# Kernel optimization log

Measured on AMD Instinct MI355X. Metric: run time of the kernel, lower is better.

Reference implementation:

```python
import jax, jax.numpy as jnp
import numpy as np

K = 3    # kernel size
PAD = 1  # padding ('same' for stride 1)


def _quantize(t):
    # dynamic per-tensor absmax int8 quantization
    s = jnp.max(jnp.abs(t)) / 127.0
    q = jnp.clip(jnp.round(t / s), -128, 127).astype(jnp.int32)
    return q, s


def _patches(x, k, pad):
    # im2col: [B,C,H,W] -> [B, C*k*k, OH, OW] (flatten order C, kh, kw matches
    # weight.reshape(Cout, Cin*k*k)); stride 1.
    B, C, H, W = x.shape
    xp = jnp.pad(x, ((0, 0), (0, 0), (pad, pad), (pad, pad)))
    cols = [xp[:, :, i:i + H, j:j + W] for i in range(k) for j in range(k)]
    return jnp.stack(cols, axis=2).reshape(B, C * k * k, H, W)


def setup_inputs() -> dict:
    key = jax.random.key(0)
    k1, k2, k3 = jax.random.split(key, 3)
    B, Cin, H, W, Cout = 8, 64, 14, 14, 64
    x = jax.random.normal(k1, (B, Cin, H, W), dtype=jnp.float32)
    weight = jax.random.normal(k2, (Cout, Cin, K, K), dtype=jnp.float32) * 0.05
    bias = jax.random.normal(k3, (Cout,), dtype=jnp.float32) * 0.1
    # LUT of the (approximate) int8 multiplier: lut[a+128, b+128] ~= a*b
    q = jnp.arange(256, dtype=jnp.float32) - 128.0
    lut = q[:, None] * q[None, :]                                   # [256,256]
    # gradient LUT: [...,0] = d(prod)/da ~= b ; [...,1] = d(prod)/db ~= a
    gradient_lut = jnp.stack(
        [jnp.broadcast_to(q[None, :], (256, 256)),
         jnp.broadcast_to(q[:, None], (256, 256))], axis=-1)        # [256,256,2]
    return {"x": x, "weight": weight, "bias": bias,
            "lut": lut, "gradient_lut": gradient_lut}


def reference(x, weight, bias, lut, gradient_lut):
    Cout = weight.shape[0]
    p = _patches(x, K, PAD)                  # [B, Kdim, OH, OW]
    qx, sx = _quantize(p)
    qw, sw = _quantize(weight.reshape(Cout, -1))   # [Cout, Kdim]
    # per-tap LUT lookup: idx[b,o,k,oh,ow] = (qx+128)*256 + (qw+128)
    idx = (qx + 128)[:, None] * 256 + (qw + 128)[None, :, :, None, None]
    vals = lut.reshape(-1)[idx]              # [B, Cout, Kdim, OH, OW]
    out = sx * sw * vals.sum(axis=2) + bias[None, :, None, None]
    return out
```

## Files before the change

### kernel.cpp

```cpp
#include <hip/hip_runtime.h>

#define NB   8
#define CIN  64
#define HW   14
#define COUT 64
#define NX   (NB*CIN*HW*HW)
#define NW   (COUT*CIN*9)


__global__ __launch_bounds__(256) void absmax_kernel(const float* __restrict__ x,
                                                     const float* __restrict__ w,
                                                     float* __restrict__ part) {
    const int bid = blockIdx.x, tid = threadIdx.x;
    float m = 0.f;
    if (bid < 64) {
        const float4* p = (const float4*)x;
        for (int i = bid * 256 + tid; i < NX / 4; i += 64 * 256) {
            float4 v = p[i];
            m = fmaxf(m, fmaxf(fmaxf(fabsf(v.x), fabsf(v.y)),
                               fmaxf(fabsf(v.z), fabsf(v.w))));
        }
    } else {
        const float4* p = (const float4*)w;
        for (int i = (bid - 64) * 256 + tid; i < NW / 4; i += 16 * 256) {
            float4 v = p[i];
            m = fmaxf(m, fmaxf(fmaxf(fabsf(v.x), fabsf(v.y)),
                               fmaxf(fabsf(v.z), fabsf(v.w))));
        }
    }
    #pragma unroll
    for (int off = 32; off; off >>= 1)
        m = fmaxf(m, __shfl_down(m, off, 64));
    __shared__ float lds[4];
    if ((tid & 63) == 0) lds[tid >> 6] = m;
    __syncthreads();
    if (tid == 0)
        part[bid] = fmaxf(fmaxf(lds[0], lds[1]), fmaxf(lds[2], lds[3]));
}

__device__ __forceinline__ float reduce_part(const float* __restrict__ part, int lo, int hi) {
    float m = 0.f;
    for (int i = lo; i < hi; ++i) m = fmaxf(m, part[i]);
    return m;
}

__device__ __forceinline__ signed char quant1(float v, float s) {
    int q = (int)rintf(v / s);
    return (signed char)min(127, max(-128, q));
}

__device__ __forceinline__ int dot4(int a, int b, int acc) {
#if __has_builtin(__builtin_amdgcn_sdot4)
    return __builtin_amdgcn_sdot4(a, b, acc, false);
#else
    acc += (int)(signed char)(a)       * (int)(signed char)(b);
    acc += (int)(signed char)(a >> 8)  * (int)(signed char)(b >> 8);
    acc += (int)(signed char)(a >> 16) * (int)(signed char)(b >> 16);
    acc += (a >> 24)                   * (b >> 24);
    return acc;
#endif
}

__global__ __launch_bounds__(512) void fused_kernel(const float* __restrict__ x,
                                                    const float* __restrict__ w,
                                                    const float* __restrict__ part,
                                                    const float* __restrict__ bias,
                                                    float* __restrict__ out) {
    __shared__ int qx_d[256 * 17];
    __shared__ int qw_i[2 * 9 * 16];
    char* qxl = (char*)qx_d;
    char* qwl = (char*)qw_i;

    const int tid = threadIdx.x;
    const int img = blockIdx.x >> 5;
    const int o0  = (blockIdx.x & 31) * 2;

    const float sx = reduce_part(part, 0, 64) / 127.0f;
    const float sw = reduce_part(part, 64, 80) / 127.0f;

    #pragma unroll
    for (int k = 0; k < 9; ++k) {
        int i = tid + k * 512;
        if (i < 256 * 17) qx_d[i] = 0;
    }
    __syncthreads();

    const float4* xb = (const float4*)(x + img * (CIN * HW * HW));
    #pragma unroll
    for (int k = 0; k < 7; ++k) {
        int i = tid + k * 512;
        if (i < 3136) {
            float4 v = xb[i];
            const float vv[4] = {v.x, v.y, v.z, v.w};
            #pragma unroll
            for (int e = 0; e < 4; ++e) {
                int idx = i * 4 + e;
                int c = idx / 196, r = idx - c * 196;
                int h = r / 14,  ww = r - h * 14;
                qxl[((h + 1) * 16 + (ww + 1)) * 68 + c] = quant1(vv[e], sx);
            }
        }
    }
    if (tid < 288) {
        float4 v = ((const float4*)w)[o0 * 144 + tid];
        const float vv[4] = {v.x, v.y, v.z, v.w};
        #pragma unroll
        for (int e = 0; e < 4; ++e) {
            int j = tid * 4 + e;
            int ol = j / 576, r2 = j - ol * 576;
            int c = r2 / 9, tap = r2 - c * 9;
            qwl[((ol * 9 + tap) * 64) + c] = quant1(vv[e], sw);
        }
    }
    __syncthreads();

    if (tid < 392) {
        const int ol = (tid >= 196) ? 1 : 0;
        const int px = tid - ol * 196;
        const int h = px / 14, ww = px - h * 14;
        int a0 = 0, a1 = 0, a2 = 0, a3 = 0;
        #pragma unroll
        for (int kh = 0; kh < 3; ++kh) {
            #pragma unroll
            for (int kw = 0; kw < 3; ++kw) {
                const int* xr = qx_d + ((h + kh) * 16 + (ww + kw)) * 17;
                const int4* wr = ((const int4*)qw_i) + (ol * 9 + kh * 3 + kw) * 4;
                int4 w0 = wr[0], w1 = wr[1], w2 = wr[2], w3 = wr[3];
                a0 = dot4(xr[0],  w0.x, a0); a1 = dot4(xr[1],  w0.y, a1);
                a2 = dot4(xr[2],  w0.z, a2); a3 = dot4(xr[3],  w0.w, a3);
                a0 = dot4(xr[4],  w1.x, a0); a1 = dot4(xr[5],  w1.y, a1);
                a2 = dot4(xr[6],  w1.z, a2); a3 = dot4(xr[7],  w1.w, a3);
                a0 = dot4(xr[8],  w2.x, a0); a1 = dot4(xr[9],  w2.y, a1);
                a2 = dot4(xr[10], w2.z, a2); a3 = dot4(xr[11], w2.w, a3);
                a0 = dot4(xr[12], w3.x, a0); a1 = dot4(xr[13], w3.y, a1);
                a2 = dot4(xr[14], w3.z, a2); a3 = dot4(xr[15], w3.w, a3);
            }
        }
        const int acc = (a0 + a1) + (a2 + a3);
        const int oc = o0 + ol;
        out[(img * 64 + oc) * 196 + px] = (sx * sw) * (float)acc + bias[oc];
    }
}

extern "C" void kernel_launch(void* const* d_in, const int* in_sizes, int n_in,
                              void* d_out, int out_size, void* d_ws, size_t ws_size,
                              hipStream_t stream) {
    const float* x    = (const float*)d_in[0];
    const float* w    = (const float*)d_in[1];
    const float* bias = (const float*)d_in[2];
    float* part = (float*)d_ws;
    float* out  = (float*)d_out;

    absmax_kernel<<<80,  256, 0, stream>>>(x, w, part);
    fused_kernel <<<256, 512, 0, stream>>>(x, w, part, bias, out);
}
```

Before: 72.32 us.

## Fuse absmax reduction into conv kernel with redundant per-block scans

Removes the separate absmax kernel launch: each block now scans the whole input and weight tensors itself to compute the quantization scales. Blocks are made coarser (8 output channels per block, 64 blocks instead of 256), so fewer blocks repeat the full-tensor scan. This trades a kernel launch and a global round-trip for redundant reads of about 400KB of x per block and less parallelism across the GPU.

```diff
diff --git a/kernel.cpp b/kernel.cpp
--- a/kernel.cpp
+++ b/kernel.cpp
@@ -6,43 +6,6 @@
 #define COUT 64
 #define NX   (NB*CIN*HW*HW)
 #define NW   (COUT*CIN*9)
-
-
-__global__ __launch_bounds__(256) void absmax_kernel(const float* __restrict__ x,
-                                                     const float* __restrict__ w,
-                                                     float* __restrict__ part) {
-    const int bid = blockIdx.x, tid = threadIdx.x;
-    float m = 0.f;
-    if (bid < 64) {
-        const float4* p = (const float4*)x;
-        for (int i = bid * 256 + tid; i < NX / 4; i += 64 * 256) {
-            float4 v = p[i];
-            m = fmaxf(m, fmaxf(fmaxf(fabsf(v.x), fabsf(v.y)),
-                               fmaxf(fabsf(v.z), fabsf(v.w))));
-        }
-    } else {
-        const float4* p = (const float4*)w;
-        for (int i = (bid - 64) * 256 + tid; i < NW / 4; i += 16 * 256) {
-            float4 v = p[i];
-            m = fmaxf(m, fmaxf(fmaxf(fabsf(v.x), fabsf(v.y)),
-                               fmaxf(fabsf(v.z), fabsf(v.w))));
-        }
-    }
-    #pragma unroll
-    for (int off = 32; off; off >>= 1)
-        m = fmaxf(m, __shfl_down(m, off, 64));
-    __shared__ float lds[4];
-    if ((tid & 63) == 0) lds[tid >> 6] = m;
-    __syncthreads();
-    if (tid == 0)
-        part[bid] = fmaxf(fmaxf(lds[0], lds[1]), fmaxf(lds[2], lds[3]));
-}
-
-__device__ __forceinline__ float reduce_part(const float* __restrict__ part, int lo, int hi) {
-    float m = 0.f;
-    for (int i = lo; i < hi; ++i) m = fmaxf(m, part[i]);
-    return m;
-}
 
 __device__ __forceinline__ signed char quant1(float v, float s) {
     int q = (int)rintf(v / s);
@@ -63,26 +26,51 @@
 
 __global__ __launch_bounds__(512) void fused_kernel(const float* __restrict__ x,
                                                     const float* __restrict__ w,
-                                                    const float* __restrict__ part,
                                                     const float* __restrict__ bias,
                                                     float* __restrict__ out) {
-    __shared__ int qx_d[256 * 17];
-    __shared__ int qw_i[2 * 9 * 16];
+    __shared__ int   qx_d[256 * 17];
+    __shared__ int   qw_i[8 * 9 * 16];
+    __shared__ float wmx[8], wmw[8];
     char* qxl = (char*)qx_d;
     char* qwl = (char*)qw_i;
 
     const int tid = threadIdx.x;
-    const int img = blockIdx.x >> 5;
-    const int o0  = (blockIdx.x & 31) * 2;
+    const int img = blockIdx.x >> 3;
+    const int o0  = (blockIdx.x & 7) * 8;
 
-    const float sx = reduce_part(part, 0, 64) / 127.0f;
-    const float sw = reduce_part(part, 64, 80) / 127.0f;
-
+    float mx = 0.f, mw = 0.f;
+    {
+        const float4* px4 = (const float4*)x;
+        for (int i = tid; i < NX / 4; i += 512) {
+            float4 v = px4[i];
+            mx = fmaxf(mx, fmaxf(fmaxf(fabsf(v.x), fabsf(v.y)),
+                                 fmaxf(fabsf(v.z), fabsf(v.w))));
+        }
+        const float4* pw4 = (const float4*)w;
+        for (int i = tid; i < NW / 4; i += 512) {
+            float4 v = pw4[i];
+            mw = fmaxf(mw, fmaxf(fmaxf(fabsf(v.x), fabsf(v.y)),
+                                 fmaxf(fabsf(v.z), fabsf(v.w))));
+        }
+        #pragma unroll
+        for (int off = 32; off; off >>= 1) {
+            mx = fmaxf(mx, __shfl_down(mx, off, 64));
+            mw = fmaxf(mw, __shfl_down(mw, off, 64));
+        }
+        if ((tid & 63) == 0) { wmx[tid >> 6] = mx; wmw[tid >> 6] = mw; }
+    }
     #pragma unroll
     for (int k = 0; k < 9; ++k) {
         int i = tid + k * 512;
         if (i < 256 * 17) qx_d[i] = 0;
     }
+    __syncthreads();
+    mx = wmx[0]; mw = wmw[0];
+    #pragma unroll
+    for (int k = 1; k < 8; ++k) {
+        mx = fmaxf(mx, wmx[k]); mw = fmaxf(mw, wmw[k]);
+    }
+    const float sx = mx / 127.0f, sw = mw / 127.0f;
     __syncthreads();
 
     const float4* xb = (const float4*)(x + img * (CIN * HW * HW));
@@ -101,22 +89,27 @@
             }
         }
     }
-    if (tid < 288) {
-        float4 v = ((const float4*)w)[o0 * 144 + tid];
-        const float vv[4] = {v.x, v.y, v.z, v.w};
-        #pragma unroll
-        for (int e = 0; e < 4; ++e) {
-            int j = tid * 4 + e;
-            int ol = j / 576, r2 = j - ol * 576;
-            int c = r2 / 9, tap = r2 - c * 9;
-            qwl[((ol * 9 + tap) * 64) + c] = quant1(vv[e], sw);
+    #pragma unroll
+    for (int k = 0; k < 3; ++k) {
+        int j4 = tid + k * 512;
+        if (j4 < 1152) {
+            float4 v = ((const float4*)w)[o0 * 144 + j4];
+            const float vv[4] = {v.x, v.y, v.z, v.w};
+            #pragma unroll
+            for (int e = 0; e < 4; ++e) {
+                int j = j4 * 4 + e;
+                int ol = j / 576, r2 = j - ol * 576;
+                int c = r2 / 9, tap = r2 - c * 9;
+                qwl[((ol * 9 + tap) * 64) + c] = quant1(vv[e], sw);
+            }
         }
     }
     __syncthreads();
 
-    if (tid < 392) {
-        const int ol = (tid >= 196) ? 1 : 0;
-        const int px = tid - ol * 196;
+    const float s = sx * sw;
+    for (int it = tid; it < 8 * 196; it += 512) {
+        const int ol = it / 196;
+        const int px = it - ol * 196;
         const int h = px / 14, ww = px - h * 14;
         int a0 = 0, a1 = 0, a2 = 0, a3 = 0;
         #pragma unroll
@@ -138,7 +131,7 @@
         }
         const int acc = (a0 + a1) + (a2 + a3);
         const int oc = o0 + ol;
-        out[(img * 64 + oc) * 196 + px] = (sx * sw) * (float)acc + bias[oc];
+        out[(img * 64 + oc) * 196 + px] = s * (float)acc + bias[oc];
     }
 }
 
@@ -148,9 +141,8 @@
     const float* x    = (const float*)d_in[0];
     const float* w    = (const float*)d_in[1];
     const float* bias = (const float*)d_in[2];
-    float* part = (float*)d_ws;
-    float* out  = (float*)d_out;
+    float* out = (float*)d_out;
+    (void)d_ws; (void)ws_size;
 
-    absmax_kernel<<<80,  256, 0, stream>>>(x, w, part);
-    fused_kernel <<<256, 512, 0, stream>>>(x, w, part, bias, out);
+    fused_kernel<<<64, 512, 0, stream>>>(x, w, bias, out);
 }
```

Result: slower. 84.98 us (+17.5%).
